# Optimization experiments

Measured on AMD Instinct MI355X. Metric: run time of the kernel, lower is better.

## Reference

```python
import jax, jax.numpy as jnp
import numpy as np

NBINS = 256

def _rescale_0_1(img):
    return (img + 1.0) * (127.0 / 255.0)

def _rescale_back(img):
    return img * (255.0 / 127.0) - 1.0

def _rgb_to_yuv_y(img):
    # tf.image.rgb_to_yuv luma coefficients; only Y channel is used downstream
    return img[..., 0] * 0.299 + img[..., 1] * 0.587 + img[..., 2] * 0.114

def _equalize_histogram(image):
    # tf.histogram_fixed_width over [0,1] with 256 bins (values clipped to range)
    idx = jnp.clip((image * NBINS).astype(jnp.int32), 0, NBINS - 1)
    hist = jnp.zeros((NBINS,), jnp.int32).at[idx.reshape(-1)].add(1)
    cdf = jnp.cumsum(hist)
    cdf_min = jnp.min(cdf)
    pix_cnt = image.shape[0] * image.shape[1]
    return (cdf - cdf_min).astype(jnp.float32) / jnp.float32(pix_cnt - 1)

def _interpolate(dx, dy, x):
    # brute-force searchsorted substitute: first index where dx - x > 0
    del_vals = dx[jnp.newaxis, :] - x[:, jnp.newaxis]          # [N, 256]
    ind_1 = jnp.argmax(jnp.sign(del_vals), axis=1)             # first positive
    ind_0 = jnp.clip(ind_1 - 1, 0, NBINS - 1)
    dx0, dx1 = dx[ind_0], dx[ind_1]
    dy0, dy1 = dy[ind_0], dy[ind_1]
    denom = dx1 - dx0
    safe_denom = jnp.where(denom == 0, jnp.float32(1.0), denom)
    interp = dy0 + (dy1 - dy0) * (x - dx0) / safe_denom
    return jnp.where(x <= dx[0], dy[0], jnp.where(x >= dx[-1], dy[-1], interp))

def setup_inputs() -> dict:
    key = jax.random.key(0)
    k1, k2 = jax.random.split(key)
    H, W = 1024, 1024
    src = jax.random.uniform(k1, (H, W, 3), jnp.float32, minval=-1.0, maxval=1.0)
    tgt = jax.random.uniform(k2, (H, W, 3), jnp.float32, minval=-1.0, maxval=1.0)
    return {"src": src, "tgt": tgt}

def reference(src, tgt):
    src = _rescale_0_1(src)
    tgt = _rescale_0_1(tgt)
    tgt_y = _rgb_to_yuv_y(tgt)
    h, w = src.shape[0], src.shape[1]
    floating_space = jnp.clip(jnp.arange(0.0, 1.00001, 1.0 / 255.0, dtype=jnp.float32), 0.0, 1.0)
    source = src[:, :, 0]
    cdfsrc = _equalize_histogram(source)
    cdftgt = _equalize_histogram(tgt_y)
    pxmap = _interpolate(cdftgt, floating_space, cdfsrc)
    pxmap = _interpolate(floating_space, pxmap, source.reshape(h * w))
    pxmap = pxmap.reshape(h, w, 1)
    res = jnp.clip(pxmap, 0.0, 1.0)
    return _rescale_back(res)
```

## Files before the change

### kernel.cpp

```cpp
#include <hip/hip_runtime.h>

#define NBINS 256

__device__ __forceinline__ float fs_val(int j) {
    const float c = (float)(1.0 / 255.0);
    float v = (float)j * c;
    return v > 1.0f ? 1.0f : v;
}

__device__ __forceinline__ int bin_of(float s) {
    int i = (int)(s * 256.0f);
    i = i < 0 ? 0 : i;
    i = i > NBINS - 1 ? NBINS - 1 : i;
    return i;
}

__global__ void hm_hist(const float* __restrict__ src,
                        const float* __restrict__ tgt,
                        int* __restrict__ histS, int* __restrict__ histT,
                        int nquad) {
    __shared__ int hs[NBINS];
    __shared__ int ht[NBINS];
    for (int i = threadIdx.x; i < NBINS; i += blockDim.x) { hs[i] = 0; ht[i] = 0; }
    __syncthreads();

    const float c1 = (float)(127.0 / 255.0);
    int tid = blockIdx.x * blockDim.x + threadIdx.x;
    int stride = gridDim.x * blockDim.x;

    for (int q = tid; q < nquad; q += stride) {
        const float4* s4 = (const float4*)(src + 12 * (size_t)q);
        float4 a = s4[0], b = s4[1], c = s4[2];
        float p0 = (a.x + 1.0f) * c1;
        float p1 = (a.w + 1.0f) * c1;
        float p2 = (b.z + 1.0f) * c1;
        float p3 = (c.y + 1.0f) * c1;
        atomicAdd(&hs[bin_of(p0)], 1);
        atomicAdd(&hs[bin_of(p1)], 1);
        atomicAdd(&hs[bin_of(p2)], 1);
        atomicAdd(&hs[bin_of(p3)], 1);

        const float4* t4 = (const float4*)(tgt + 12 * (size_t)q);
        float4 ta = t4[0], tb = t4[1], tc = t4[2];
        {
            float r = (ta.x + 1.0f) * c1, g = (ta.y + 1.0f) * c1, bb = (ta.z + 1.0f) * c1;
            float y = r * 0.299f + g * 0.587f + bb * 0.114f;
            atomicAdd(&ht[bin_of(y)], 1);
        }
        {
            float r = (ta.w + 1.0f) * c1, g = (tb.x + 1.0f) * c1, bb = (tb.y + 1.0f) * c1;
            float y = r * 0.299f + g * 0.587f + bb * 0.114f;
            atomicAdd(&ht[bin_of(y)], 1);
        }
        {
            float r = (tb.z + 1.0f) * c1, g = (tb.w + 1.0f) * c1, bb = (tc.x + 1.0f) * c1;
            float y = r * 0.299f + g * 0.587f + bb * 0.114f;
            atomicAdd(&ht[bin_of(y)], 1);
        }
        {
            float r = (tc.y + 1.0f) * c1, g = (tc.z + 1.0f) * c1, bb = (tc.w + 1.0f) * c1;
            float y = r * 0.299f + g * 0.587f + bb * 0.114f;
            atomicAdd(&ht[bin_of(y)], 1);
        }
    }
    __syncthreads();
    for (int i = threadIdx.x; i < NBINS; i += blockDim.x) {
        if (hs[i]) atomicAdd(&histS[i], hs[i]);
        if (ht[i]) atomicAdd(&histT[i], ht[i]);
    }
}

__global__ void hm_scan_apply(const float* __restrict__ src,
                              const int* __restrict__ histS,
                              const int* __restrict__ histT,
                              float* __restrict__ out, int nquad, int npix) {
    __shared__ int sS[NBINS];
    __shared__ int sT[NBINS];
    __shared__ float cdfT[NBINS];
    __shared__ float pm[NBINS];

    const int t = threadIdx.x;
    sS[t] = histS[t];
    sT[t] = histT[t];
    __syncthreads();
    for (int off = 1; off < NBINS; off <<= 1) {
        int vS = sS[t], vT = sT[t];
        int aS = (t >= off) ? sS[t - off] : 0;
        int aT = (t >= off) ? sT[t - off] : 0;
        __syncthreads();
        sS[t] = vS + aS;
        sT[t] = vT + aT;
        __syncthreads();
    }
    int minS = sS[0], minT = sT[0];
    float denomN = (float)(npix - 1);
    float xS = (float)(sS[t] - minS) / denomN;
    cdfT[t] = (float)(sT[t] - minT) / denomN;
    __syncthreads();

    float res;
    if (xS <= cdfT[0]) {
        res = fs_val(0);
    } else if (xS >= cdfT[NBINS - 1]) {
        res = fs_val(NBINS - 1);
    } else {
        int lo = 0, hi = NBINS - 1;
        while (hi - lo > 1) {
            int mid = (lo + hi) >> 1;
            if (cdfT[mid] > xS) hi = mid; else lo = mid;
        }
        int j1 = hi, j0 = hi - 1;
        float dx0 = cdfT[j0], dx1 = cdfT[j1];
        float dy0 = fs_val(j0), dy1 = fs_val(j1);
        res = dy0 + (dy1 - dy0) * (xS - dx0) / (dx1 - dx0);
    }
    pm[t] = res;
    __syncthreads();

    const float c1 = (float)(127.0 / 255.0);
    const float c2 = (float)(255.0 / 127.0);
    int tid = blockIdx.x * blockDim.x + threadIdx.x;
    int stride = gridDim.x * blockDim.x;

    for (int q = tid; q < nquad; q += stride) {
        const float4* s4 = (const float4*)(src + 12 * (size_t)q);
        float4 a = s4[0], b = s4[1], c = s4[2];
        float xv[4] = {a.x, a.w, b.z, c.y};
        float ov[4];
        #pragma unroll
        for (int k = 0; k < 4; ++k) {
            float x = (xv[k] + 1.0f) * c1;
            float r;
            if (x <= 0.0f) {
                r = pm[0];
            } else if (x >= 1.0f) {
                r = pm[NBINS - 1];
            } else {
                int g = (int)(x * 255.0f) + 1;
                g = g < 1 ? 1 : (g > NBINS - 1 ? NBINS - 1 : g);
                while (g < NBINS - 1 && fs_val(g) <= x) ++g;
                while (g > 1 && fs_val(g - 1) > x) --g;
                int j1 = g, j0 = g - 1;
                float dx0 = fs_val(j0), dx1 = fs_val(j1);
                r = pm[j0] + (pm[j1] - pm[j0]) * (x - dx0) / (dx1 - dx0);
            }
            r = r < 0.0f ? 0.0f : (r > 1.0f ? 1.0f : r);
            ov[k] = r * c2 - 1.0f;
        }
        float4 o;
        o.x = ov[0]; o.y = ov[1]; o.z = ov[2]; o.w = ov[3];
        ((float4*)out)[q] = o;
    }
}

extern "C" void kernel_launch(void* const* d_in, const int* in_sizes, int n_in,
                              void* d_out, int out_size, void* d_ws, size_t ws_size,
                              hipStream_t stream) {
    const float* src = (const float*)d_in[0];
    const float* tgt = (const float*)d_in[1];
    float* out = (float*)d_out;

    int npix = out_size;
    int nquad = npix >> 2;

    int* histS = (int*)d_ws;
    int* histT = histS + NBINS;

    hipMemsetAsync(d_ws, 0, 2 * NBINS * sizeof(int), stream);

    hm_hist<<<512, 512, 0, stream>>>(src, tgt, histS, histT, nquad);

    hm_scan_apply<<<1024, 256, 0, stream>>>(src, histS, histT, out, nquad, npix);
}
```

Measured before the change: 88.33 us.

## Replace global histogram atomics with per-block partials and single-block reduce-scan

The histogram kernel now writes per-block partial histograms instead of atomically adding into a global histogram, which also removes the memset. A new single-block kernel reduces the partials, scans them and computes the 256-entry pixel map once, instead of every apply block redoing the scan. The apply kernel then only loads the precomputed map and runs one thread per quad. This adds a third launch and a serial single-block stage, and the histogram pass drops to fewer blocks.

```diff
diff --git a/kernel.cpp b/kernel.cpp
--- a/kernel.cpp
+++ b/kernel.cpp
@@ -1,6 +1,7 @@
 #include <hip/hip_runtime.h>
 
 #define NBINS 256
+#define HIST_BLOCKS 256
 
 __device__ __forceinline__ float fs_val(int j) {
     const float c = (float)(1.0 / 255.0);
@@ -17,15 +18,16 @@
 
 __global__ void hm_hist(const float* __restrict__ src,
                         const float* __restrict__ tgt,
-                        int* __restrict__ histS, int* __restrict__ histT,
+                        int* __restrict__ partS, int* __restrict__ partT,
                         int nquad) {
     __shared__ int hs[NBINS];
     __shared__ int ht[NBINS];
-    for (int i = threadIdx.x; i < NBINS; i += blockDim.x) { hs[i] = 0; ht[i] = 0; }
+    const int t = threadIdx.x;
+    if (t < NBINS) { hs[t] = 0; ht[t] = 0; }
     __syncthreads();
 
     const float c1 = (float)(127.0 / 255.0);
-    int tid = blockIdx.x * blockDim.x + threadIdx.x;
+    int tid = blockIdx.x * blockDim.x + t;
     int stride = gridDim.x * blockDim.x;
 
     for (int q = tid; q < nquad; q += stride) {
@@ -64,57 +66,86 @@
         }
     }
     __syncthreads();
-    for (int i = threadIdx.x; i < NBINS; i += blockDim.x) {
-        if (hs[i]) atomicAdd(&histS[i], hs[i]);
-        if (ht[i]) atomicAdd(&histT[i], ht[i]);
-    }
-}
-
-__global__ void hm_scan_apply(const float* __restrict__ src,
-                              const int* __restrict__ histS,
-                              const int* __restrict__ histT,
-                              float* __restrict__ out, int nquad, int npix) {
+    if (t < NBINS) partS[blockIdx.x * NBINS + t] = hs[t];
+    else           partT[blockIdx.x * NBINS + (t - NBINS)] = ht[t - NBINS];
+}
+
+__global__ void hm_reduce_scan(const int* __restrict__ partS,
+                               const int* __restrict__ partT,
+                               float* __restrict__ pm, int npix) {
+    __shared__ int redS[4][NBINS];
+    __shared__ int redT[4][NBINS];
     __shared__ int sS[NBINS];
     __shared__ int sT[NBINS];
     __shared__ float cdfT[NBINS];
+
+    const int t = threadIdx.x;
+    const int bin = t & (NBINS - 1);
+    const int chunk = t >> 8;
+
+    int accS = 0, accT = 0;
+    const int b0 = chunk * (HIST_BLOCKS / 4);
+    #pragma unroll 8
+    for (int b = b0; b < b0 + HIST_BLOCKS / 4; ++b) {
+        accS += partS[b * NBINS + bin];
+        accT += partT[b * NBINS + bin];
+    }
+    redS[chunk][bin] = accS;
+    redT[chunk][bin] = accT;
+    __syncthreads();
+
+    if (t < NBINS) {
+        sS[t] = redS[0][t] + redS[1][t] + redS[2][t] + redS[3][t];
+        sT[t] = redT[0][t] + redT[1][t] + redT[2][t] + redT[3][t];
+    }
+    __syncthreads();
+
+    for (int off = 1; off < NBINS; off <<= 1) {
+        int vS = 0, vT = 0, aS = 0, aT = 0;
+        if (t < NBINS) {
+            vS = sS[t]; vT = sT[t];
+            if (t >= off) { aS = sS[t - off]; aT = sT[t - off]; }
+        }
+        __syncthreads();
+        if (t < NBINS) { sS[t] = vS + aS; sT[t] = vT + aT; }
+        __syncthreads();
+    }
+
+    float denomN = (float)(npix - 1);
+    float xS = 0.0f;
+    if (t < NBINS) {
+        int minS = sS[0], minT = sT[0];
+        xS = (float)(sS[t] - minS) / denomN;
+        cdfT[t] = (float)(sT[t] - minT) / denomN;
+    }
+    __syncthreads();
+
+    if (t < NBINS) {
+        float res;
+        if (xS <= cdfT[0]) {
+            res = fs_val(0);
+        } else if (xS >= cdfT[NBINS - 1]) {
+            res = fs_val(NBINS - 1);
+        } else {
+            int lo = 0, hi = NBINS - 1;
+            while (hi - lo > 1) {
+                int mid = (lo + hi) >> 1;
+                if (cdfT[mid] > xS) hi = mid; else lo = mid;
+            }
+            int j1 = hi, j0 = hi - 1;
+            float dx0 = cdfT[j0], dx1 = cdfT[j1];
+            float dy0 = fs_val(j0), dy1 = fs_val(j1);
+            res = dy0 + (dy1 - dy0) * (xS - dx0) / (dx1 - dx0);
+        }
+        pm[t] = res;
+    }
+}
+
+__global__ void hm_apply(const float* __restrict__ src,
+                         const float* __restrict__ pxmap,
+                         float* __restrict__ out, int nquad) {
     __shared__ float pm[NBINS];
-
-    const int t = threadIdx.x;
-    sS[t] = histS[t];
-    sT[t] = histT[t];
-    __syncthreads();
-    for (int off = 1; off < NBINS; off <<= 1) {
-        int vS = sS[t], vT = sT[t];
-        int aS = (t >= off) ? sS[t - off] : 0;
-        int aT = (t >= off) ? sT[t - off] : 0;
-        __syncthreads();
-        sS[t] = vS + aS;
-        sT[t] = vT + aT;
-        __syncthreads();
-    }
-    int minS = sS[0], minT = sT[0];
-    float denomN = (float)(npix - 1);
-    float xS = (float)(sS[t] - minS) / denomN;
-    cdfT[t] = (float)(sT[t] - minT) / denomN;
-    __syncthreads();
-
-    float res;
-    if (xS <= cdfT[0]) {
-        res = fs_val(0);
-    } else if (xS >= cdfT[NBINS - 1]) {
-        res = fs_val(NBINS - 1);
-    } else {
-        int lo = 0, hi = NBINS - 1;
-        while (hi - lo > 1) {
-            int mid = (lo + hi) >> 1;
-            if (cdfT[mid] > xS) hi = mid; else lo = mid;
-        }
-        int j1 = hi, j0 = hi - 1;
-        float dx0 = cdfT[j0], dx1 = cdfT[j1];
-        float dy0 = fs_val(j0), dy1 = fs_val(j1);
-        res = dy0 + (dy1 - dy0) * (xS - dx0) / (dx1 - dx0);
-    }
-    pm[t] = res;
+    for (int i = threadIdx.x; i < NBINS; i += blockDim.x) pm[i] = pxmap[i];
     __syncthreads();
 
     const float c1 = (float)(127.0 / 255.0);
@@ -163,12 +194,14 @@
     int npix = out_size;
     int nquad = npix >> 2;
 
-    int* histS = (int*)d_ws;
-    int* histT = histS + NBINS;
-
-    hipMemsetAsync(d_ws, 0, 2 * NBINS * sizeof(int), stream);
-
-    hm_hist<<<512, 512, 0, stream>>>(src, tgt, histS, histT, nquad);
-
-    hm_scan_apply<<<1024, 256, 0, stream>>>(src, histS, histT, out, nquad, npix);
-}
+    int* partS = (int*)d_ws;
+    int* partT = partS + HIST_BLOCKS * NBINS;
+    float* pm  = (float*)(partT + HIST_BLOCKS * NBINS);
+
+    hm_hist<<<HIST_BLOCKS, 512, 0, stream>>>(src, tgt, partS, partT, nquad);
+
+    hm_reduce_scan<<<1, 1024, 0, stream>>>(partS, partT, pm, npix);
+
+    int blocks = (nquad + 255) / 256;
+    hm_apply<<<blocks, 256, 0, stream>>>(src, pm, out, nquad);
+}
```

Result: faster. 85.73 us (-2.9%).
